# Performance work log

Hardware: AMD Instinct MI355X
Metric: run time of the kernel (lower is better)

Reference implementation:

```python
import jax, jax.numpy as jnp
import numpy as np

N = 4_194_304

def setup_inputs() -> dict:
    key = jax.random.key(0)
    k1, k2 = jax.random.split(key)
    preds = jax.random.normal(k1, (N, 5), dtype=jnp.float32)
    target = jax.random.normal(k2, (N, 3), dtype=jnp.float32)
    return {"preds": preds, "target": target}

def reference(preds, target):
    # main MSE on first 3 columns: [N, 3]
    main_mse = (preds[:, :3] - target[:, :3]) ** 2

    p2 = preds[:, 2]
    p3 = preds[:, 3]
    p4 = preds[:, 4]
    t2 = target[:, 2]

    # lower-range loss (note: original multiplies by 2**2 == 4, not squares, in first branch)
    lower = jnp.where(
        p3 > p2,
        (p4 - t2) * 4.0,
        jnp.where(p3 > t2 * 0.95, 0.0, (p3 - t2 * 0.95) ** 2),
    )
    # upper-range loss
    upper = jnp.where(
        p4 < p2,
        (p4 - t2) * 4.0,
        jnp.where(p4 < t2 * 1.05, 0.0, (p4 - t2 * 1.05) ** 2),
    )

    loss = jnp.concatenate([main_mse, lower[:, None], upper[:, None]], axis=1)  # [N, 5]
    return jnp.mean(loss)
```

## Files before the change

### kernel.cpp

```cpp
#include <hip/hip_runtime.h>


#define BLOCK 256
#define NBLK  1024
#define WAVES_PER_BLOCK (BLOCK / 64)

__device__ __forceinline__ float row_loss(float p0, float p1, float p2,
                                          float p3, float p4,
                                          float t0, float t1, float t2) {
    float d0 = p0 - t0, d1 = p1 - t1, d2 = p2 - t2;
    float acc = d0 * d0 + d1 * d1 + d2 * d2;
    float tl = t2 * 0.95f;
    float tu = t2 * 1.05f;
    float pen = (p4 - t2) * 4.0f;
    float dl = p3 - tl;
    float du = p4 - tu;
    float lower = (p3 > p2) ? pen : ((p3 > tl) ? 0.0f : dl * dl);
    float upper = (p4 < p2) ? pen : ((p4 < tu) ? 0.0f : du * du);
    return acc + lower + upper;
}

__global__ __launch_bounds__(BLOCK) void ql_main(const float* __restrict__ preds,
                                                 const float* __restrict__ target,
                                                 double* __restrict__ ws,
                                                 long ntiles) {
    __shared__ float4 sbuf[WAVES_PER_BLOCK][128];
    __shared__ double wsum[WAVES_PER_BLOCK];

    const int lane = threadIdx.x & 63;
    const int w = threadIdx.x >> 6;
    const long gwave = (long)blockIdx.x * WAVES_PER_BLOCK + w;
    const long nw = (long)gridDim.x * WAVES_PER_BLOCK;

    const float4* pb4 = (const float4*)preds;
    const float4* tb4 = (const float4*)target;
    float* sp = (float*)&sbuf[w][0];
    float* st = (float*)&sbuf[w][80];

    float acc = 0.0f;
    long t = gwave;
    bool have = t < ntiles;
    float4 r0, r1;
    if (have) {
        r0 = pb4[t * 80 + lane];
        r1 = (lane < 16) ? pb4[t * 80 + 64 + lane] : tb4[t * 48 + (lane - 16)];
    }

    while (have) {
        sbuf[w][lane] = r0;
        sbuf[w][(lane < 16) ? (64 + lane) : (80 + lane - 16)] = r1;

        long tn = t + nw;
        bool haven = tn < ntiles;
        if (haven) {
            r0 = pb4[tn * 80 + lane];
            r1 = (lane < 16) ? pb4[tn * 80 + 64 + lane] : tb4[tn * 48 + (lane - 16)];
        }

        acc += row_loss(sp[5 * lane + 0], sp[5 * lane + 1], sp[5 * lane + 2],
                        sp[5 * lane + 3], sp[5 * lane + 4],
                        st[3 * lane + 0], st[3 * lane + 1], st[3 * lane + 2]);

        t = tn;
        have = haven;
    }

    double dacc = (double)acc;
#pragma unroll
    for (int off = 32; off > 0; off >>= 1)
        dacc += __shfl_down(dacc, off, 64);
    if (lane == 0) wsum[w] = dacc;
    __syncthreads();
    if (threadIdx.x == 0)
        ws[blockIdx.x] = wsum[0] + wsum[1] + wsum[2] + wsum[3];
}

__global__ __launch_bounds__(256) void ql_finalize(const double* __restrict__ ws,
                                                   const float* __restrict__ preds,
                                                   const float* __restrict__ target,
                                                   float* __restrict__ out,
                                                   long rows, long tail_start) {
    __shared__ double wsum[4];
    const int tid = threadIdx.x;

    double d = 0.0;
#pragma unroll
    for (int i = 0; i < NBLK / 256; ++i)
        d += ws[tid + i * 256];

    long r = tail_start + tid;
    if (r < rows) {
        const float* p = preds + r * 5;
        const float* tg = target + r * 3;
        d += (double)row_loss(p[0], p[1], p[2], p[3], p[4], tg[0], tg[1], tg[2]);
    }

#pragma unroll
    for (int off = 32; off > 0; off >>= 1)
        d += __shfl_down(d, off, 64);
    int lane = tid & 63, w = tid >> 6;
    if (lane == 0) wsum[w] = d;
    __syncthreads();
    if (tid == 0) {
        double total = wsum[0] + wsum[1] + wsum[2] + wsum[3];
        out[0] = (float)(total / ((double)rows * 5.0));
    }
}

extern "C" void kernel_launch(void* const* d_in, const int* in_sizes, int n_in,
                              void* d_out, int out_size, void* d_ws, size_t ws_size,
                              hipStream_t stream) {
    const float* preds = (const float*)d_in[0];
    const float* target = (const float*)d_in[1];
    long rows = (long)in_sizes[0] / 5;
    long ntiles = rows / 64;
    long tail_start = ntiles * 64;

    double* partials = (double*)d_ws;

    ql_main<<<NBLK, BLOCK, 0, stream>>>(preds, target, partials, ntiles);
    ql_finalize<<<1, 256, 0, stream>>>(partials, preds, target,
                                       (float*)d_out, rows, tail_start);
}
```

Measured before the change: 157.7 us.

## Double-buffer tile prefetch per wave and double grid size

Each wave now keeps two tiles in flight in registers and alternates between two shared-memory buffers, so more global loads are outstanding while the loss is computed. The grid also grows from 1024 to 2048 blocks, and the finalize kernel sums proportionally more partials. The aim is more memory-level parallelism on a bandwidth-bound reduction, paid for with extra registers and LDS per wave.

```diff
diff --git a/kernel.cpp b/kernel.cpp
--- a/kernel.cpp
+++ b/kernel.cpp
@@ -2,7 +2,7 @@
 
 
 #define BLOCK 256
-#define NBLK  1024
+#define NBLK  2048
 #define WAVES_PER_BLOCK (BLOCK / 64)
 
 __device__ __forceinline__ float row_loss(float p0, float p1, float p2,
@@ -24,7 +24,7 @@
                                                  const float* __restrict__ target,
                                                  double* __restrict__ ws,
                                                  long ntiles) {
-    __shared__ float4 sbuf[WAVES_PER_BLOCK][128];
+    __shared__ float4 sbuf[WAVES_PER_BLOCK][2][128];
     __shared__ double wsum[WAVES_PER_BLOCK];
 
     const int lane = threadIdx.x & 63;
@@ -34,35 +34,68 @@
 
     const float4* pb4 = (const float4*)preds;
     const float4* tb4 = (const float4*)target;
-    float* sp = (float*)&sbuf[w][0];
-    float* st = (float*)&sbuf[w][80];
+
+    float* sp0 = (float*)&sbuf[w][0][0];
+    float* st0 = (float*)&sbuf[w][0][80];
+    float* sp1 = (float*)&sbuf[w][1][0];
+    float* st1 = (float*)&sbuf[w][1][80];
+
+    const int slot = (lane < 16) ? (64 + lane) : (80 + (lane - 16));
 
     float acc = 0.0f;
-    long t = gwave;
-    bool have = t < ntiles;
-    float4 r0, r1;
-    if (have) {
-        r0 = pb4[t * 80 + lane];
-        r1 = (lane < 16) ? pb4[t * 80 + 64 + lane] : tb4[t * 48 + (lane - 16)];
+
+    long ta = gwave;
+    long tb = gwave + nw;
+    bool ha = ta < ntiles;
+    bool hb = tb < ntiles;
+    float4 a0, a1, b0, b1;
+    if (ha) {
+        a0 = pb4[ta * 80 + lane];
+        const float4* s = (lane < 16) ? (pb4 + ta * 80 + 64 + lane)
+                                      : (tb4 + ta * 48 + (lane - 16));
+        a1 = *s;
+    }
+    if (hb) {
+        b0 = pb4[tb * 80 + lane];
+        const float4* s = (lane < 16) ? (pb4 + tb * 80 + 64 + lane)
+                                      : (tb4 + tb * 48 + (lane - 16));
+        b1 = *s;
     }
 
-    while (have) {
-        sbuf[w][lane] = r0;
-        sbuf[w][(lane < 16) ? (64 + lane) : (80 + lane - 16)] = r1;
+    while (ha) {
+        sbuf[w][0][lane] = a0;
+        sbuf[w][0][slot] = a1;
+        long tn = ta + 2 * nw;
+        bool hn = tn < ntiles;
+        if (hn) {
+            a0 = pb4[tn * 80 + lane];
+            const float4* s = (lane < 16) ? (pb4 + tn * 80 + 64 + lane)
+                                          : (tb4 + tn * 48 + (lane - 16));
+            a1 = *s;
+        }
+        acc += row_loss(sp0[5 * lane + 0], sp0[5 * lane + 1], sp0[5 * lane + 2],
+                        sp0[5 * lane + 3], sp0[5 * lane + 4],
+                        st0[3 * lane + 0], st0[3 * lane + 1], st0[3 * lane + 2]);
+        ta = tn;
 
-        long tn = t + nw;
-        bool haven = tn < ntiles;
-        if (haven) {
-            r0 = pb4[tn * 80 + lane];
-            r1 = (lane < 16) ? pb4[tn * 80 + 64 + lane] : tb4[tn * 48 + (lane - 16)];
+        if (!hb) break;
+
+        sbuf[w][1][lane] = b0;
+        sbuf[w][1][slot] = b1;
+        long tm = tb + 2 * nw;
+        bool hm = tm < ntiles;
+        if (hm) {
+            b0 = pb4[tm * 80 + lane];
+            const float4* s = (lane < 16) ? (pb4 + tm * 80 + 64 + lane)
+                                          : (tb4 + tm * 48 + (lane - 16));
+            b1 = *s;
         }
-
-        acc += row_loss(sp[5 * lane + 0], sp[5 * lane + 1], sp[5 * lane + 2],
-                        sp[5 * lane + 3], sp[5 * lane + 4],
-                        st[3 * lane + 0], st[3 * lane + 1], st[3 * lane + 2]);
-
-        t = tn;
-        have = haven;
+        acc += row_loss(sp1[5 * lane + 0], sp1[5 * lane + 1], sp1[5 * lane + 2],
+                        sp1[5 * lane + 3], sp1[5 * lane + 4],
+                        st1[3 * lane + 0], st1[3 * lane + 1], st1[3 * lane + 2]);
+        tb = tm;
+        hb = hm;
+        ha = hn;
     }
 
     double dacc = (double)acc;
```

Result: no change. 160.8 us (+2.0%).

## Replace LDS staging with per-thread 4-row register groups and nontemporal loads

Applied to the files above, without the earlier changes.

Each thread now loads four rows at a time as five float4s of preds and three float4s of target, then computes the losses directly from registers. This removes the shared-memory transpose and the software double-buffering. Loads are marked nontemporal and the grid doubles to 2048 blocks. The per-thread loads stride across 80/48 bytes between lanes, so each load instruction is less coalesced, which may raise memory transaction overhead. The finalize kernel still reads NBLK/256 partials per thread, so it stays consistent with the new block count.

```diff
diff --git a/kernel.cpp b/kernel.cpp
--- a/kernel.cpp
+++ b/kernel.cpp
@@ -2,8 +2,9 @@
 
 
 #define BLOCK 256
-#define NBLK  1024
-#define WAVES_PER_BLOCK (BLOCK / 64)
+#define NBLK  2048
+
+typedef float f4 __attribute__((ext_vector_type(4)));
 
 __device__ __forceinline__ float row_loss(float p0, float p1, float p2,
                                           float p3, float p4,
@@ -23,52 +24,39 @@
 __global__ __launch_bounds__(BLOCK) void ql_main(const float* __restrict__ preds,
                                                  const float* __restrict__ target,
                                                  double* __restrict__ ws,
-                                                 long ntiles) {
-    __shared__ float4 sbuf[WAVES_PER_BLOCK][128];
-    __shared__ double wsum[WAVES_PER_BLOCK];
+                                                 long ngroups) {
+    __shared__ double wsum[BLOCK / 64];
 
-    const int lane = threadIdx.x & 63;
-    const int w = threadIdx.x >> 6;
-    const long gwave = (long)blockIdx.x * WAVES_PER_BLOCK + w;
-    const long nw = (long)gridDim.x * WAVES_PER_BLOCK;
-
-    const float4* pb4 = (const float4*)preds;
-    const float4* tb4 = (const float4*)target;
-    float* sp = (float*)&sbuf[w][0];
-    float* st = (float*)&sbuf[w][80];
+    const f4* pb4 = (const f4*)preds;
+    const f4* tb4 = (const f4*)target;
+    const long T = (long)gridDim.x * BLOCK;
 
     float acc = 0.0f;
-    long t = gwave;
-    bool have = t < ntiles;
-    float4 r0, r1;
-    if (have) {
-        r0 = pb4[t * 80 + lane];
-        r1 = (lane < 16) ? pb4[t * 80 + 64 + lane] : tb4[t * 48 + (lane - 16)];
-    }
 
-    while (have) {
-        sbuf[w][lane] = r0;
-        sbuf[w][(lane < 16) ? (64 + lane) : (80 + lane - 16)] = r1;
+    for (long g = (long)blockIdx.x * BLOCK + threadIdx.x; g < ngroups; g += T) {
+        const f4* p = pb4 + g * 5;
+        const f4* q = tb4 + g * 3;
+        f4 r0 = __builtin_nontemporal_load(p + 0);
+        f4 r1 = __builtin_nontemporal_load(p + 1);
+        f4 r2 = __builtin_nontemporal_load(p + 2);
+        f4 r3 = __builtin_nontemporal_load(p + 3);
+        f4 r4 = __builtin_nontemporal_load(p + 4);
+        f4 s0 = __builtin_nontemporal_load(q + 0);
+        f4 s1 = __builtin_nontemporal_load(q + 1);
+        f4 s2 = __builtin_nontemporal_load(q + 2);
 
-        long tn = t + nw;
-        bool haven = tn < ntiles;
-        if (haven) {
-            r0 = pb4[tn * 80 + lane];
-            r1 = (lane < 16) ? pb4[tn * 80 + 64 + lane] : tb4[tn * 48 + (lane - 16)];
-        }
-
-        acc += row_loss(sp[5 * lane + 0], sp[5 * lane + 1], sp[5 * lane + 2],
-                        sp[5 * lane + 3], sp[5 * lane + 4],
-                        st[3 * lane + 0], st[3 * lane + 1], st[3 * lane + 2]);
-
-        t = tn;
-        have = haven;
+        acc += row_loss(r0.x, r0.y, r0.z, r0.w, r1.x, s0.x, s0.y, s0.z);
+        acc += row_loss(r1.y, r1.z, r1.w, r2.x, r2.y, s0.w, s1.x, s1.y);
+        acc += row_loss(r2.z, r2.w, r3.x, r3.y, r3.z, s1.z, s1.w, s2.x);
+        acc += row_loss(r3.w, r4.x, r4.y, r4.z, r4.w, s2.y, s2.z, s2.w);
     }
 
     double dacc = (double)acc;
 #pragma unroll
     for (int off = 32; off > 0; off >>= 1)
         dacc += __shfl_down(dacc, off, 64);
+    const int lane = threadIdx.x & 63;
+    const int w = threadIdx.x >> 6;
     if (lane == 0) wsum[w] = dacc;
     __syncthreads();
     if (threadIdx.x == 0)
@@ -113,12 +101,12 @@
     const float* preds = (const float*)d_in[0];
     const float* target = (const float*)d_in[1];
     long rows = (long)in_sizes[0] / 5;
-    long ntiles = rows / 64;
-    long tail_start = ntiles * 64;
+    long ngroups = rows / 4;
+    long tail_start = ngroups * 4;
 
     double* partials = (double*)d_ws;
 
-    ql_main<<<NBLK, BLOCK, 0, stream>>>(preds, target, partials, ntiles);
+    ql_main<<<NBLK, BLOCK, 0, stream>>>(preds, target, partials, ngroups);
     ql_finalize<<<1, 256, 0, stream>>>(partials, preds, target,
                                        (float*)d_out, rows, tail_start);
 }
```

New measurement: 167.5 us. +6.2%, slower.
